# Kernel tuning notes

Measured on AMD Instinct MI355X. Metric: run time of the kernel, lower is better.

Reference implementation:

```python
import jax, jax.numpy as jnp
import numpy as np

D_MODEL = 1024
NUM_HEADS = 16
WINDOW = 256
HEAD_DIM = D_MODEL // NUM_HEADS


def setup_inputs() -> dict:
    key = jax.random.key(0)
    ks = jax.random.split(key, 5)
    B, L, D = 2, 2048, D_MODEL
    s = 1.0 / np.sqrt(D)
    x = jax.random.normal(ks[0], (B, L, D), dtype=jnp.float32)
    w_qkv = jax.random.normal(ks[1], (3 * D, D), dtype=jnp.float32) * s
    b_qkv = jnp.zeros((3 * D,), dtype=jnp.float32)
    w_proj = jax.random.normal(ks[2], (D, D), dtype=jnp.float32) * s
    b_proj = jnp.zeros((D,), dtype=jnp.float32)
    return {"x": x, "w_qkv": w_qkv, "b_qkv": b_qkv, "w_proj": w_proj, "b_proj": b_proj}


def reference(x, w_qkv, b_qkv, w_proj, b_proj):
    B, L, D = x.shape
    H, E = NUM_HEADS, HEAD_DIM
    scale = 1.0 / jnp.sqrt(jnp.asarray(E, dtype=x.dtype))
    # torch Linear: y = x @ W.T + b
    qkv = (x @ w_qkv.T + b_qkv).reshape(B, L, 3, H, E)
    qkv = jnp.transpose(qkv, (2, 0, 3, 1, 4))  # [3, B, H, L, E]
    q, k, v = qkv[0], qkv[1], qkv[2]
    scores = jnp.einsum('bhle,bhme->bhlm', q, k) * scale  # [B,H,L,L]
    i = jnp.arange(L)[:, None]
    j = jnp.arange(L)[None, :]
    mask = (j > i) | ((i - j) >= WINDOW)  # causal OR outside window
    scores = jnp.where(mask, jnp.asarray(-10000.0, dtype=scores.dtype), scores)
    attn = jax.nn.softmax(scores, axis=-1)
    out = jnp.einsum('bhlm,bhme->bhle', attn, v)  # [B,H,L,E]
    out = jnp.transpose(out, (0, 2, 1, 3)).reshape(B, L, D)
    return out @ w_proj.T + b_proj
```

## Files before the change

### kernel.cpp

```cpp
#include <hip/hip_runtime.h>

typedef __bf16 bf16x8 __attribute__((ext_vector_type(8)));
typedef float f32x4 __attribute__((ext_vector_type(4)));
typedef unsigned short u16;
typedef unsigned int u32;

__device__ __forceinline__ u16 f2bf(float f) {
  u32 u = __builtin_bit_cast(u32, f);
  u32 r = (u + 0x7FFFu + ((u >> 16) & 1u)) >> 16;
  return (u16)r;
}

__device__ __forceinline__ void gload16(const u16* g, u16* lds_base) {
  __builtin_amdgcn_global_load_lds(
      (const __attribute__((address_space(1))) void*)g,
      (__attribute__((address_space(3))) void*)lds_base, 16, 0, 0);
}

__global__ void cast_all(const float* __restrict__ x,  u16* __restrict__ xo,
                         const float* __restrict__ wq, u16* __restrict__ wqo,
                         const float* __restrict__ wp, u16* __restrict__ wpo) {
  const int NX = (2 * 2048 * 1024) / 4;
  const int NQ = (3072 * 1024) / 4;
  const int NP = (1024 * 1024) / 4;
  int i = blockIdx.x * blockDim.x + threadIdx.x;
  int stride = gridDim.x * blockDim.x;
  for (; i < NX + NQ + NP; i += stride) {
    const float4* s; uint2* d; int j;
    if (i < NX)            { s = (const float4*)x;  d = (uint2*)xo;  j = i; }
    else if (i < NX + NQ)  { s = (const float4*)wq; d = (uint2*)wqo; j = i - NX; }
    else                   { s = (const float4*)wp; d = (uint2*)wpo; j = i - NX - NQ; }
    float4 f = s[j];
    uint2 o;
    o.x = (u32)f2bf(f.x) | ((u32)f2bf(f.y) << 16);
    o.y = (u32)f2bf(f.z) | ((u32)f2bf(f.w) << 16);
    d[j] = o;
  }
}

__global__ __launch_bounds__(512, 2) void gemm256(
    const u16* __restrict__ A, const u16* __restrict__ W,
    const float* __restrict__ bias, u16* __restrict__ Cout,
    int M, int N, int K)
{
  __shared__ u16 Alds[2][256][64];
  __shared__ u16 Blds[2][256][64];
  const int tid  = threadIdx.x;
  const int lane = tid & 63;
  const int wave = tid >> 6;
  const int wm128 = (wave >> 2) * 128;
  const int wn64  = (wave & 3) * 64;
  const int quad = lane >> 4;
  const int li   = lane & 15;
  const int swz  = (li & 7) * 8;

  const int b = blockIdx.x;
  const int wgid = (b & 7) * 24 + (b >> 3);
  const int m0 = (wgid & 15) * 256;
  const int n0 = (wgid >> 4) * 256;

  const int srow = lane >> 3;
  const int sblk = (lane & 7) ^ srow;
  const u16* gaBase = A + (size_t)(m0 + wave * 32 + srow) * K + sblk * 8;
  const u16* gbBase = W + (size_t)(n0 + wave * 32 + srow) * K + sblk * 8;

  auto stage = [&](int buf, int k0) {
#pragma unroll
    for (int c = 0; c < 4; ++c)
      gload16(gaBase + (size_t)(c * 8) * K + k0, &Alds[buf][wave * 32 + c * 8][0]);
#pragma unroll
    for (int c = 0; c < 4; ++c)
      gload16(gbBase + (size_t)(c * 8) * K + k0, &Blds[buf][wave * 32 + c * 8][0]);
  };

  f32x4 acc[8][4] = {};
  const int NT16 = K >> 6;

  stage(0, 0);
  asm volatile("s_waitcnt vmcnt(0)" ::: "memory");
  __builtin_amdgcn_s_barrier();

  for (int t = 0; t < NT16; ++t) {
    const int buf = t & 1;
    bf16x8 bfr[4][2];
#pragma unroll
    for (int sp = 0; sp < 4; ++sp) {
      bf16x8 af[2][2];
#pragma unroll
      for (int mi = 0; mi < 2; ++mi)
#pragma unroll
        for (int k = 0; k < 2; ++k)
          af[mi][k] = *(const bf16x8*)
              &Alds[buf][wm128 + (2 * sp + mi) * 16 + li][(quad * 8 + k * 32) ^ swz];
      if (sp == 0) {
#pragma unroll
        for (int nf = 0; nf < 4; ++nf)
#pragma unroll
          for (int k = 0; k < 2; ++k)
            bfr[nf][k] = *(const bf16x8*)
                &Blds[buf][wn64 + nf * 16 + li][(quad * 8 + k * 32) ^ swz];
        if (t + 1 < NT16) stage(buf ^ 1, (t + 1) * 64);
      }
      __builtin_amdgcn_s_barrier();
      asm volatile("s_waitcnt lgkmcnt(0)" ::: "memory");
      __builtin_amdgcn_sched_barrier(0);
      __builtin_amdgcn_s_setprio(1);
#pragma unroll
      for (int mi = 0; mi < 2; ++mi)
#pragma unroll
        for (int nf = 0; nf < 4; ++nf)
#pragma unroll
          for (int k = 0; k < 2; ++k)
            acc[2 * sp + mi][nf] = __builtin_amdgcn_mfma_f32_16x16x32_bf16(
                af[mi][k], bfr[nf][k], acc[2 * sp + mi][nf], 0, 0, 0);
      __builtin_amdgcn_s_setprio(0);
      if (sp == 3) asm volatile("s_waitcnt vmcnt(0)" ::: "memory");
      __builtin_amdgcn_s_barrier();
    }
  }

#pragma unroll
  for (int nf = 0; nf < 4; ++nf) {
    int gn = n0 + wn64 + nf * 16 + li;
    float bv = bias[gn];
#pragma unroll
    for (int mf = 0; mf < 8; ++mf) {
#pragma unroll
      for (int r = 0; r < 4; ++r) {
        int gm = m0 + wm128 + mf * 16 + quad * 4 + r;
        Cout[(size_t)gm * N + gn] = f2bf(acc[mf][nf][r] + bv);
      }
    }
  }
}

template<int OUT_BF16, int BM, int BN>
__global__ __launch_bounds__(256) void gemm_nt(
    const u16* __restrict__ A, const u16* __restrict__ W,
    const float* __restrict__ bias, void* __restrict__ Cout,
    int M, int N, int K)
{
  constexpr int MT = BM / 32;
  constexpr int NT = BN / 32;
  __shared__ u16 Alds[2][BM][32];
  __shared__ u16 Blds[2][BN][32];
  const int tid  = threadIdx.x;
  const int lane = tid & 63;
  const int wave = tid >> 6;
  const int wm = (wave >> 1) * (BM / 2);
  const int wn = (wave & 1) * (BN / 2);

  const int b    = blockIdx.x;
  const int xcd  = b & 7;
  const int slot = b >> 3;
  const int npx  = (N / BN) >> 3;
  const int m0 = (slot / npx) * BM;
  const int n0 = (xcd * npx + slot % npx) * BN;

  const int quad = lane >> 4;
  const int li   = lane & 15;

  const u16* ga = &A[(size_t)(m0 + wave * (BM / 4) + (lane >> 2)) * K + (lane & 3) * 8];
  const u16* gb = &W[(size_t)(n0 + wave * (BN / 4) + (lane >> 2)) * K + (lane & 3) * 8];

  auto stage = [&](int buf, int k0) {
#pragma unroll
    for (int i = 0; i < BM / 64; i++)
      gload16(ga + (size_t)i * 16 * K + k0, &Alds[buf][wave * (BM / 4) + i * 16][0]);
#pragma unroll
    for (int i = 0; i < BN / 64; i++)
      gload16(gb + (size_t)i * 16 * K + k0, &Blds[buf][wave * (BN / 4) + i * 16][0]);
  };

  f32x4 acc[MT][NT] = {};
  const int niter = K / 32;

  stage(0, 0);

#pragma unroll 2
  for (int kt = 0; kt < niter; kt++) {
    __syncthreads();
    if (kt + 1 < niter) stage((kt + 1) & 1, (kt + 1) * 32);
    const int buf = kt & 1;
    bf16x8 af[MT], bfr[NT];
#pragma unroll
    for (int t = 0; t < MT; t++)
      af[t] = *(const bf16x8*)&Alds[buf][wm + t * 16 + li][quad * 8];
#pragma unroll
    for (int t = 0; t < NT; t++)
      bfr[t] = *(const bf16x8*)&Blds[buf][wn + t * 16 + li][quad * 8];
#pragma unroll
    for (int mt = 0; mt < MT; mt++)
#pragma unroll
      for (int nt = 0; nt < NT; nt++)
        acc[mt][nt] = __builtin_amdgcn_mfma_f32_16x16x32_bf16(af[mt], bfr[nt], acc[mt][nt], 0, 0, 0);
  }

#pragma unroll
  for (int mt = 0; mt < MT; mt++)
#pragma unroll
    for (int nt = 0; nt < NT; nt++) {
      int gn = n0 + wn + nt * 16 + li;
      float bv = bias[gn];
#pragma unroll
      for (int r = 0; r < 4; r++) {
        int gm = m0 + wm + mt * 16 + quad * 4 + r;
        float v = acc[mt][nt][r] + bv;
        if (OUT_BF16)
          ((u16*)Cout)[(size_t)gm * N + gn] = f2bf(v);
        else
          ((float*)Cout)[(size_t)gm * N + gn] = v;
      }
    }
}

__global__ __launch_bounds__(256, 4) void attn_kernel(const u16* __restrict__ qkv,
                                                      u16* __restrict__ aout)
{
  const int L = 2048, DQ = 3072, D = 1024;
  const int q0 = blockIdx.x * 64;
  const int h  = blockIdx.y;
  const int b  = blockIdx.z;
  const int tid  = threadIdx.x;
  const int lane = tid & 63;
  const int wave = tid >> 6;
  const int quad = lane >> 4;
  const int li   = lane & 15;

  __shared__ u16 Klds[64][68];
  __shared__ u16 Vt[64][68];
  __shared__ u16 Plds[4][16][68];

  const u16* base = qkv + (size_t)b * L * DQ + h * 64;

  bf16x8 qf[2];
  {
    const u16* qsrc = base + (size_t)(q0 + wave * 16 + li) * DQ;
    qf[0] = *(const bf16x8*)&qsrc[quad * 8];
    qf[1] = *(const bf16x8*)&qsrc[32 + quad * 8];
  }

  f32x4 O[4] = {};
  float lsum[4] = {0.f, 0.f, 0.f, 0.f};

  const float scale = 0.125f;
  const int gq = q0 + wave * 16 + quad * 4;

  const int sr2 = (tid >> 3) * 2, sc = (tid & 7) * 8;
  const u16* ksbase = base + D;
  const u16* vsbase = base + 2 * D;
  uint4 kr0, kr1, vr0, vr1;
  auto loadkv = [&](int t) {
    int kb = q0 - 256 + t * 64;
    const u16* ks = ksbase + (size_t)kb * DQ;
    const u16* vs = vsbase + (size_t)kb * DQ;
    kr0 = *(const uint4*)&ks[(size_t)sr2 * DQ + sc];
    kr1 = *(const uint4*)&ks[(size_t)(sr2 + 1) * DQ + sc];
    vr0 = *(const uint4*)&vs[(size_t)sr2 * DQ + sc];
    vr1 = *(const uint4*)&vs[(size_t)(sr2 + 1) * DQ + sc];
  };

  const int t0 = (blockIdx.x < 4) ? (4 - (int)blockIdx.x) : 0;
  loadkv(t0);

  for (int t = t0; t < 5; t++) {
    const int kb = q0 - 256 + t * 64;
    __syncthreads();
    *(uint4*)&Klds[sr2][sc]     = kr0;
    *(uint4*)&Klds[sr2 + 1][sc] = kr1;
    {
      u32 a0[4] = {vr0.x, vr0.y, vr0.z, vr0.w};
      u32 a1[4] = {vr1.x, vr1.y, vr1.z, vr1.w};
#pragma unroll
      for (int j2 = 0; j2 < 4; j2++) {
        u32 lo0 = a0[j2] & 0xffffu, hi0 = a0[j2] >> 16;
        u32 lo1 = a1[j2] & 0xffffu, hi1 = a1[j2] >> 16;
        *(u32*)&Vt[sc + 2 * j2][sr2]     = lo0 | (lo1 << 16);
        *(u32*)&Vt[sc + 2 * j2 + 1][sr2] = hi0 | (hi1 << 16);
      }
    }
    __syncthreads();
    if (t + 1 < 5) loadkv(t + 1);

    f32x4 sacc[4] = {};
#pragma unroll
    for (int nt = 0; nt < 4; nt++) {
      bf16x8 kf0 = *(const bf16x8*)&Klds[nt * 16 + li][quad * 8];
      bf16x8 kf1 = *(const bf16x8*)&Klds[nt * 16 + li][32 + quad * 8];
      sacc[nt] = __builtin_amdgcn_mfma_f32_16x16x32_bf16(qf[0], kf0, sacc[nt], 0, 0, 0);
      sacc[nt] = __builtin_amdgcn_mfma_f32_16x16x32_bf16(qf[1], kf1, sacc[nt], 0, 0, 0);
    }

#pragma unroll
    for (int nt = 0; nt < 4; nt++) {
      int gj = kb + nt * 16 + li;
#pragma unroll
      for (int r = 0; r < 4; r++) {
        bool masked = (gj > gq + r) || ((gq + r) - gj >= 256);
        float p = masked ? 0.f : __expf(sacc[nt][r] * scale - 12.f);
        lsum[r] += p;
        Plds[wave][quad * 4 + r][nt * 16 + li] = f2bf(p);
      }
    }

    bf16x8 pf0 = *(const bf16x8*)&Plds[wave][li][quad * 8];
    bf16x8 pf1 = *(const bf16x8*)&Plds[wave][li][32 + quad * 8];
#pragma unroll
    for (int nt = 0; nt < 4; nt++) {
      bf16x8 vb0 = *(const bf16x8*)&Vt[nt * 16 + li][quad * 8];
      bf16x8 vb1 = *(const bf16x8*)&Vt[nt * 16 + li][32 + quad * 8];
      O[nt] = __builtin_amdgcn_mfma_f32_16x16x32_bf16(pf0, vb0, O[nt], 0, 0, 0);
      O[nt] = __builtin_amdgcn_mfma_f32_16x16x32_bf16(pf1, vb1, O[nt], 0, 0, 0);
    }
  }

#pragma unroll
  for (int d = 1; d < 16; d <<= 1)
#pragma unroll
    for (int r = 0; r < 4; r++)
      lsum[r] += __shfl_xor(lsum[r], d, 64);
#pragma unroll
  for (int r = 0; r < 4; r++) {
    float inv = 1.f / lsum[r];
#pragma unroll
    for (int nt = 0; nt < 4; nt++)
      aout[(size_t)(b * L + gq + r) * D + h * 64 + nt * 16 + li] = f2bf(O[nt][r] * inv);
  }
}

extern "C" void kernel_launch(void* const* d_in, const int* in_sizes, int n_in,
                              void* d_out, int out_size, void* d_ws, size_t ws_size,
                              hipStream_t stream) {
  const float* x      = (const float*)d_in[0];
  const float* w_qkv  = (const float*)d_in[1];
  const float* b_qkv  = (const float*)d_in[2];
  const float* w_proj = (const float*)d_in[3];
  const float* b_proj = (const float*)d_in[4];
  float* out = (float*)d_out;

  char* ws = (char*)d_ws;
  u16* x_bf     = (u16*)(ws);
  u16* wqkv_bf  = (u16*)(ws + ((size_t)8  << 20));
  u16* wproj_bf = (u16*)(ws + ((size_t)14 << 20));
  u16* qkv_bf   = (u16*)(ws + ((size_t)16 << 20));
  u16* attn_bf  = (u16*)(ws + ((size_t)40 << 20));

  cast_all<<<1024, 256, 0, stream>>>(x, x_bf, w_qkv, wqkv_bf, w_proj, wproj_bf);

  gemm256<<<(4096 / 256) * (3072 / 256), 512, 0, stream>>>(
      x_bf, wqkv_bf, b_qkv, qkv_bf, 4096, 3072, 1024);

  attn_kernel<<<dim3(2048 / 64, 16, 2), 256, 0, stream>>>(qkv_bf, attn_bf);

  gemm_nt<0, 128, 64><<<(4096 / 128) * (1024 / 64), 256, 0, stream>>>(
      attn_bf, wproj_bf, b_proj, out, 4096, 1024, 1024);
}
```

Baseline: 167.2 us.

## Triple-buffer QKV GEMM with K=32 stages and split A/B loads; widen proj tile

```diff
diff --git a/kernel.cpp b/kernel.cpp
--- a/kernel.cpp
+++ b/kernel.cpp
@@ -43,8 +43,8 @@
     const float* __restrict__ bias, u16* __restrict__ Cout,
     int M, int N, int K)
 {
-  __shared__ u16 Alds[2][256][64];
-  __shared__ u16 Blds[2][256][64];
+  __shared__ u16 Alds[3][128][64];
+  __shared__ u16 Blds[3][128][64];
   const int tid  = threadIdx.x;
   const int lane = tid & 63;
   const int wave = tid >> 6;
@@ -52,71 +52,84 @@
   const int wn64  = (wave & 3) * 64;
   const int quad = lane >> 4;
   const int li   = lane & 15;
-  const int swz  = (li & 7) * 8;
 
   const int b = blockIdx.x;
   const int wgid = (b & 7) * 24 + (b >> 3);
   const int m0 = (wgid & 15) * 256;
   const int n0 = (wgid >> 4) * 256;
 
-  const int srow = lane >> 3;
-  const int sblk = (lane & 7) ^ srow;
-  const u16* gaBase = A + (size_t)(m0 + wave * 32 + srow) * K + sblk * 8;
-  const u16* gbBase = W + (size_t)(n0 + wave * 32 + srow) * K + sblk * 8;
-
-  auto stage = [&](int buf, int k0) {
-#pragma unroll
-    for (int c = 0; c < 4; ++c)
-      gload16(gaBase + (size_t)(c * 8) * K + k0, &Alds[buf][wave * 32 + c * 8][0]);
-#pragma unroll
-    for (int c = 0; c < 4; ++c)
-      gload16(gbBase + (size_t)(c * 8) * K + k0, &Blds[buf][wave * 32 + c * 8][0]);
+  const int b7   = (lane & 7) ^ (lane >> 3);
+  const int rloc = 2 * (lane >> 3) + (b7 >> 2);
+  const int kloc = (b7 & 3) * 8;
+  const u16* gaL = A + (size_t)(m0 + wave * 32 + rloc) * K + kloc;
+  const u16* gbL = W + (size_t)(n0 + wave * 32 + rloc) * K + kloc;
+
+  auto stageA = [&](int s, int k0) {
+#pragma unroll
+    for (int c = 0; c < 2; ++c)
+      gload16(gaL + (size_t)(c * 16) * K + k0, &Alds[s][wave * 16 + c * 8][0]);
+  };
+  auto stageB = [&](int s, int k0) {
+#pragma unroll
+    for (int c = 0; c < 2; ++c)
+      gload16(gbL + (size_t)(c * 16) * K + k0, &Blds[s][wave * 16 + c * 8][0]);
+  };
+
+  auto frag = [&](const u16* base, int m) -> bf16x8 {
+    int line = m >> 1;
+    int blk  = (((m & 1) << 2) + quad) ^ (line & 7);
+    return *(const bf16x8*)(base + line * 64 + blk * 8);
   };
 
   f32x4 acc[8][4] = {};
-  const int NT16 = K >> 6;
-
-  stage(0, 0);
-  asm volatile("s_waitcnt vmcnt(0)" ::: "memory");
+  const int NU = K >> 5;
+
+  stageA(0, 0);  stageB(0, 0);
+  stageA(1, 32); stageB(1, 32);
+  asm volatile("s_waitcnt vmcnt(4)" ::: "memory");
   __builtin_amdgcn_s_barrier();
 
-  for (int t = 0; t < NT16; ++t) {
-    const int buf = t & 1;
-    bf16x8 bfr[4][2];
-#pragma unroll
-    for (int sp = 0; sp < 4; ++sp) {
-      bf16x8 af[2][2];
-#pragma unroll
-      for (int mi = 0; mi < 2; ++mi)
-#pragma unroll
-        for (int k = 0; k < 2; ++k)
-          af[mi][k] = *(const bf16x8*)
-              &Alds[buf][wm128 + (2 * sp + mi) * 16 + li][(quad * 8 + k * 32) ^ swz];
-      if (sp == 0) {
-#pragma unroll
-        for (int nf = 0; nf < 4; ++nf)
-#pragma unroll
-          for (int k = 0; k < 2; ++k)
-            bfr[nf][k] = *(const bf16x8*)
-                &Blds[buf][wn64 + nf * 16 + li][(quad * 8 + k * 32) ^ swz];
-        if (t + 1 < NT16) stage(buf ^ 1, (t + 1) * 64);
-      }
-      __builtin_amdgcn_s_barrier();
-      asm volatile("s_waitcnt lgkmcnt(0)" ::: "memory");
-      __builtin_amdgcn_sched_barrier(0);
-      __builtin_amdgcn_s_setprio(1);
-#pragma unroll
-      for (int mi = 0; mi < 2; ++mi)
-#pragma unroll
-        for (int nf = 0; nf < 4; ++nf)
-#pragma unroll
-          for (int k = 0; k < 2; ++k)
-            acc[2 * sp + mi][nf] = __builtin_amdgcn_mfma_f32_16x16x32_bf16(
-                af[mi][k], bfr[nf][k], acc[2 * sp + mi][nf], 0, 0, 0);
-      __builtin_amdgcn_s_setprio(0);
-      if (sp == 3) asm volatile("s_waitcnt vmcnt(0)" ::: "memory");
-      __builtin_amdgcn_s_barrier();
-    }
+  int cu = 0, sb = 2;
+  for (int u = 0; u < NU; ++u) {
+    const u16* Ac = &Alds[cu][0][0];
+    const u16* Bc = &Blds[cu][0][0];
+    const int k2 = (u + 2) * 32;
+    bf16x8 af0[4], bfr[4];
+#pragma unroll
+    for (int f = 0; f < 4; ++f) af0[f] = frag(Ac, wm128 + f * 16 + li);
+#pragma unroll
+    for (int n = 0; n < 4; ++n) bfr[n] = frag(Bc, wn64 + n * 16 + li);
+    if (u + 2 < NU) stageA(sb, k2);
+    __builtin_amdgcn_s_barrier();
+    asm volatile("s_waitcnt lgkmcnt(0)" ::: "memory");
+    __builtin_amdgcn_sched_barrier(0);
+    __builtin_amdgcn_s_setprio(1);
+#pragma unroll
+    for (int f = 0; f < 4; ++f)
+#pragma unroll
+      for (int n = 0; n < 4; ++n)
+        acc[f][n] = __builtin_amdgcn_mfma_f32_16x16x32_bf16(af0[f], bfr[n], acc[f][n], 0, 0, 0);
+    __builtin_amdgcn_s_setprio(0);
+    __builtin_amdgcn_s_barrier();
+    bf16x8 af1[4];
+#pragma unroll
+    for (int f = 0; f < 4; ++f) af1[f] = frag(Ac, wm128 + (4 + f) * 16 + li);
+    if (u + 2 < NU) stageB(sb, k2);
+    __builtin_amdgcn_s_barrier();
+    asm volatile("s_waitcnt lgkmcnt(0)" ::: "memory");
+    __builtin_amdgcn_sched_barrier(0);
+    __builtin_amdgcn_s_setprio(1);
+#pragma unroll
+    for (int f = 0; f < 4; ++f)
+#pragma unroll
+      for (int n = 0; n < 4; ++n)
+        acc[4 + f][n] = __builtin_amdgcn_mfma_f32_16x16x32_bf16(af1[f], bfr[n], acc[4 + f][n], 0, 0, 0);
+    __builtin_amdgcn_s_setprio(0);
+    if (u + 2 < NU) asm volatile("s_waitcnt vmcnt(4)" ::: "memory");
+    else            asm volatile("s_waitcnt vmcnt(0)" ::: "memory");
+    __builtin_amdgcn_s_barrier();
+    cu = (cu == 2) ? 0 : cu + 1;
+    sb = (sb == 2) ? 0 : sb + 1;
   }
 
 #pragma unroll
@@ -352,6 +365,6 @@
 
   attn_kernel<<<dim3(2048 / 64, 16, 2), 256, 0, stream>>>(qkv_bf, attn_bf);
 
-  gemm_nt<0, 128, 64><<<(4096 / 128) * (1024 / 64), 256, 0, stream>>>(
+  gemm_nt<0, 128, 128><<<(4096 / 128) * (1024 / 128), 256, 0, stream>>>(
       attn_bf, wproj_bf, b_proj, out, 4096, 1024, 1024);
 }
```

Result: slower. 170.7 us (+2.1%).
